# Performance work log

Measured on AMD Instinct MI355X. Metric: run time of the kernel, lower is better.

## Reference

```python
import jax, jax.numpy as jnp
import numpy as np

D = 128
H = 4
DK = D // H


def _spmm(row, col, val, x, n):
    # sparse.mm(adj, x) with adj in COO form: out[row] += val * x[col]
    return jax.ops.segment_sum(val[:, None] * x[col], row, num_segments=n)


def _arrg(h, a1_w, a1_b, a2_w, a2_b):
    return jax.nn.leaky_relu(h @ a1_w + a1_b, negative_slope=0.01) @ a2_w + a2_b


def _cross_attn(x, q_x, q_w, k_w, v_w):
    n, d = x.shape
    m = q_x.shape[0]
    q = (q_x @ q_w).reshape(m, H, DK).transpose(1, 0, 2)   # [H, Q, dk]
    k = (x @ k_w).reshape(n, H, DK).transpose(1, 0, 2)     # [H, N, dk]
    v = (q_x @ v_w).reshape(m, H, DK).transpose(1, 0, 2)   # [H, Q, dk]
    s = jnp.einsum('hnd,hqd->hnq', k, q) / jnp.sqrt(jnp.float32(DK))
    w = jax.nn.softmax(s, axis=-1)                          # softmax over queries
    out = jnp.einsum('hnq,hqd->hnd', w, v).transpose(1, 0, 2).reshape(n, d)
    return out + x


def setup_inputs() -> dict:
    key = jax.random.key(0)
    ks = iter(jax.random.split(key, 64))
    nrm = lambda shape, s=0.05: jax.random.normal(next(ks), shape, jnp.float32) * s
    inp = {}
    inp['trans_w'] = nrm((1, D)); inp['trans_b'] = nrm((D,))
    inp['g_w'] = nrm((D, D));     inp['g_b'] = nrm((D,))
    inp['qg_w'] = nrm((D, D));    inp['qg_b'] = nrm((D,))
    inp['q_w'] = nrm((D, D)); inp['k_w'] = nrm((D, D)); inp['v_w'] = nrm((D, D))
    inp['a1_w'] = nrm((D, 2 * D)); inp['a1_b'] = nrm((2 * D,))
    inp['a2_w'] = nrm((2 * D, D)); inp['a2_b'] = nrm((D,))
    inp['x0'] = jax.random.normal(next(ks), (25000,), jnp.float32)
    inp['q0'] = jax.random.normal(next(ks), (100,), jnp.float32)
    for i in (1, 2, 3):
        inp[f'xin{i}'] = jax.random.normal(next(ks), (25000,), jnp.float32)
        inp[f'qin{i}'] = jax.random.normal(next(ks), (100,), jnp.float32)
    n_sizes = {1: 50000, 2: 75000, 3: 100000}
    q_sizes = {1: 200, 2: 300, 3: 400}
    for i in (1, 2, 3):
        e = 16 * n_sizes[i]
        inp[f'aval{i}'] = jax.random.uniform(next(ks), (e,), jnp.float32)
        inp[f'arow{i}'] = jax.random.randint(next(ks), (e,), 0, n_sizes[i], jnp.int64)
        inp[f'acol{i}'] = jax.random.randint(next(ks), (e,), 0, n_sizes[i], jnp.int64)
        qe = 16 * q_sizes[i]
        inp[f'qval{i}'] = jax.random.uniform(next(ks), (qe,), jnp.float32)
        inp[f'qrow{i}'] = jax.random.randint(next(ks), (qe,), 0, q_sizes[i], jnp.int64)
        inp[f'qcol{i}'] = jax.random.randint(next(ks), (qe,), 0, q_sizes[i], jnp.int64)
    return inp


def reference(trans_w, trans_b, g_w, g_b, qg_w, qg_b, q_w, k_w, v_w,
              a1_w, a1_b, a2_w, a2_b,
              x0, q0, xin1, xin2, xin3, qin1, qin2, qin3,
              aval1, aval2, aval3, qval1, qval2, qval3,
              arow1, acol1, arow2, acol2, arow3, acol3,
              qrow1, qcol1, qrow2, qcol2, qrow3, qcol3):
    trans = lambda v: v[:, None] @ trans_w + trans_b
    x = trans(x0)
    qx = trans(q0)
    steps = [
        (xin1, qin1, arow1, acol1, aval1, qrow1, qcol1, qval1, 50000, 200),
        (xin2, qin2, arow2, acol2, aval2, qrow2, qcol2, qval2, 75000, 300),
        (xin3, qin3, arow3, acol3, aval3, qrow3, qcol3, qval3, 100000, 400),
    ]
    for xin, qin, ar, ac, av, qr, qc, qv, n, m in steps:
        x = jnp.concatenate([x, trans(xin)], axis=0)
        qx = jnp.concatenate([qx, trans(qin)], axis=0)
        x = _spmm(ar, ac, av, x @ g_w + g_b, n)
        qx = _spmm(qr, qc, qv, qx @ qg_w + qg_b, m)
        x = _arrg(x, a1_w, a1_b, a2_w, a2_b)
        qx = _arrg(qx, a1_w, a1_b, a2_w, a2_b)
        x = _cross_attn(x, qx, q_w, k_w, v_w)
    return (x, qx)
```

## Files before the change

kernel.cpp:

```cpp
#include <hip/hip_runtime.h>

typedef unsigned short u16;
typedef __attribute__((ext_vector_type(8))) short bf16x8;
typedef __attribute__((ext_vector_type(4))) float f32x4;

__device__ __forceinline__ float b2f(u16 v) {
    return __uint_as_float(((unsigned)v) << 16);
}
__device__ __forceinline__ u16 f2b(float x) {
    unsigned u = __float_as_uint(x);
    unsigned r = u + 0x7FFFu + ((u >> 16) & 1u);
    return (u16)(r >> 16);
}
__device__ __forceinline__ float4 load_bf4(const u16* p) {
    ushort4 q = *(const ushort4*)p;
    float4 f;
    f.x = b2f(q.x); f.y = b2f(q.y); f.z = b2f(q.z); f.w = b2f(q.w);
    return f;
}
__device__ __forceinline__ float4 in4(const void* p, long off, bool bf) {
    if (bf) return load_bf4((const u16*)p + off);
    return *(const float4*)((const float*)p + off);
}
__device__ __forceinline__ float in1(const void* p, long off, bool bf) {
    if (bf) return b2f(((const u16*)p)[off]);
    return ((const float*)p)[off];
}
__device__ __forceinline__ int inIdx(const void* p, long i, bool i64) {
    return ((const int*)p)[i64 ? 2 * i : i];
}

__global__ void sniff_kernel(const u16* __restrict__ x0bits, const int* __restrict__ arow,
                             int* __restrict__ flags) {
    if (threadIdx.x != 0 || blockIdx.x != 0) return;
    int plaus = 0;
    for (int i = 0; i < 256; ++i) {
        u16 v = x0bits[i];
        int e = (v >> 7) & 0xFF;
        if (v == 0 || (e >= 100 && e <= 135)) plaus++;
    }
    flags[0] = (plaus >= 200) ? 1 : 0;
    int nz = 0;
    for (int i = 1; i < 128; i += 2) nz += (arow[i] != 0);
    flags[1] = (nz == 0) ? 1 : 0;
}

__global__ void trans_kernel(const void* __restrict__ v, const void* __restrict__ tw,
                             const void* __restrict__ tb, float* __restrict__ out,
                             int rows, const int* __restrict__ flags) {
    const bool bf = flags[0] != 0;
    int t = blockIdx.x * blockDim.x + threadIdx.x;
    int c4 = (t & 31) * 4;
    int r = t >> 5;
    if (r >= rows) return;
    float vv = in1(v, r, bf);
    float4 w4 = in4(tw, c4, bf);
    float4 b4 = in4(tb, c4, bf);
    float4 o;
    o.x = vv * w4.x + b4.x; o.y = vv * w4.y + b4.y;
    o.z = vv * w4.z + b4.z; o.w = vv * w4.w + b4.w;
    *(float4*)(out + (size_t)r * 128 + c4) = o;
}

__global__ void wprep_kernel(const void* __restrict__ src, u16* __restrict__ dst,
                             int K, int N, const int* __restrict__ flags) {
    const bool bf = flags[0] != 0;
    int idx = blockIdx.x * blockDim.x + threadIdx.x;
    if (idx >= K * N) return;
    int j = idx & 7, lane = (idx >> 3) & 63, t = idx >> 9;
    int KC = K >> 5;
    int kc = t % KC, ct = t / KC;
    int k = kc * 32 + (lane >> 4) * 8 + j;
    int nn = ct * 16 + (lane & 15);
    dst[idx] = f2b(in1(src, (long)k * N + nn, bf));
}

template<int KTOT, int NOUT, bool LEAKY, typename AT, typename CT>
__launch_bounds__(256)
__global__ void gemm_mfma_kernel(const AT* __restrict__ A, const u16* __restrict__ Wf,
                                 const void* __restrict__ bias, CT* __restrict__ C,
                                 int n, const int* __restrict__ flags) {
    constexpr int KC = KTOT / 32;
    constexpr int NT = NOUT / 16;
    __shared__ u16 wlds[KTOT * NOUT];
    {
        const int4* srcw = (const int4*)Wf;
        int4* dstw = (int4*)wlds;
        constexpr int NV = KTOT * NOUT * 2 / 16;
#pragma unroll
        for (int i = 0; i < NV / 256; ++i)
            dstw[i * 256 + threadIdx.x] = srcw[i * 256 + threadIdx.x];
    }
    __syncthreads();
    const bool bf = flags[0] != 0;
    const int lane = threadIdx.x & 63;
    const int wave = threadIdx.x >> 6;
    const int quad = lane >> 4, col = lane & 15;
    const int rbase = (blockIdx.x * 4 + wave) * 16;
    if (rbase >= n) return;
    int node = rbase + col; if (node >= n) node = n - 1;
    f32x4 acc[NT];
#pragma unroll
    for (int ct = 0; ct < NT; ++ct) acc[ct] = (f32x4){0.f, 0.f, 0.f, 0.f};
#pragma unroll
    for (int kc = 0; kc < KC; ++kc) {
        bf16x8 af;
        if constexpr (sizeof(AT) == 2) {
            af = *(const bf16x8*)((const u16*)A + (size_t)node * KTOT + kc * 32 + quad * 8);
        } else {
            const float* ap = (const float*)A + (size_t)node * KTOT + kc * 32 + quad * 8;
            float4 a0 = *(const float4*)ap;
            float4 a1 = *(const float4*)(ap + 4);
            af[0] = (short)f2b(a0.x); af[1] = (short)f2b(a0.y);
            af[2] = (short)f2b(a0.z); af[3] = (short)f2b(a0.w);
            af[4] = (short)f2b(a1.x); af[5] = (short)f2b(a1.y);
            af[6] = (short)f2b(a1.z); af[7] = (short)f2b(a1.w);
        }
#pragma unroll
        for (int ct = 0; ct < NT; ++ct) {
            bf16x8 wf = *(const bf16x8*)(wlds + (((ct * KC + kc) * 64 + lane) * 8));
            acc[ct] = __builtin_amdgcn_mfma_f32_16x16x32_bf16(af, wf, acc[ct], 0, 0, 0);
        }
    }
#pragma unroll
    for (int ct = 0; ct < NT; ++ct) {
        int colg = ct * 16 + col;
        float b = bias ? in1(bias, colg, bf) : 0.f;
#pragma unroll
        for (int r = 0; r < 4; ++r) {
            int row = rbase + quad * 4 + r;
            if (row >= n) continue;
            float v = acc[ct][r] + b;
            if (LEAKY) v = v > 0.f ? v : 0.01f * v;
            if constexpr (sizeof(CT) == 2) C[(size_t)row * NOUT + colg] = (CT)f2b(v);
            else                           C[(size_t)row * NOUT + colg] = (CT)v;
        }
    }
}

#define RSH 8
#define NBC_MAX 512
#define EPB 4096

__global__ void zero_int_kernel(int* __restrict__ p, int n) {
    int i = blockIdx.x * blockDim.x + threadIdx.x;
    if (i < n) p[i] = 0;
}

__global__ void bhist_kernel(const void* __restrict__ rows, int e, int* __restrict__ bcnt,
                             int nbc, const int* __restrict__ flags) {
    __shared__ int hist[NBC_MAX];
    const bool i64 = flags[1] != 0;
    for (int i = threadIdx.x; i < nbc; i += 256) hist[i] = 0;
    __syncthreads();
    int base = blockIdx.x * 8192;
    int end = base + 8192; if (end > e) end = e;
    for (int i = base + threadIdx.x; i < end; i += 256)
        atomicAdd(&hist[inIdx(rows, i, i64) >> RSH], 1);
    __syncthreads();
    for (int i = threadIdx.x; i < nbc; i += 256) {
        int c = hist[i];
        if (c) atomicAdd(&bcnt[i], c);
    }
}

__global__ void scanA_kernel(const int* __restrict__ cnt, int n, int* __restrict__ bsum) {
    int base = blockIdx.x * 2048;
    int s = 0;
    for (int j = threadIdx.x; j < 2048; j += 256) {
        int idx = base + j;
        if (idx < n) s += cnt[idx];
    }
#pragma unroll
    for (int off = 32; off; off >>= 1) s += __shfl_down(s, off);
    __shared__ int ws[4];
    if ((threadIdx.x & 63) == 0) ws[threadIdx.x >> 6] = s;
    __syncthreads();
    if (threadIdx.x == 0) bsum[blockIdx.x] = ws[0] + ws[1] + ws[2] + ws[3];
}
__global__ void scanB_kernel(int* __restrict__ bsum, int nb) {
    if (threadIdx.x == 0) {
        int acc = 0;
        for (int i = 0; i < nb; ++i) { int v = bsum[i]; bsum[i] = acc; acc += v; }
    }
}
__global__ void scanC_kernel(const int* __restrict__ cnt, int n, const int* __restrict__ bsum,
                             int* __restrict__ optr, int* __restrict__ ocur) {
    __shared__ int tsum[256];
    int base = blockIdx.x * 2048 + threadIdx.x * 8;
    int v[8]; int s = 0;
#pragma unroll
    for (int j = 0; j < 8; ++j) {
        int idx = base + j;
        v[j] = (idx < n) ? cnt[idx] : 0;
        s += v[j];
    }
    tsum[threadIdx.x] = s;
    __syncthreads();
    for (int off = 1; off < 256; off <<= 1) {
        int t = (threadIdx.x >= off) ? tsum[threadIdx.x - off] : 0;
        __syncthreads();
        tsum[threadIdx.x] += t;
        __syncthreads();
    }
    int excl = bsum[blockIdx.x] + tsum[threadIdx.x] - s;
#pragma unroll
    for (int j = 0; j < 8; ++j) {
        int idx = base + j;
        if (idx < n) { optr[idx] = excl; ocur[idx] = excl; }
        excl += v[j];
    }
}

__launch_bounds__(256)
__global__ void psort_kernel(const void* __restrict__ rows, const void* __restrict__ colsin,
                             const void* __restrict__ valsin, int e,
                             int* __restrict__ gcur, int2* __restrict__ pack0,
                             int nbc, const int* __restrict__ flags) {
    __shared__ int hist[NBC_MAX];
    __shared__ int scan[NBC_MAX];
    __shared__ int base[NBC_MAX];
    __shared__ int cur[NBC_MAX];
    __shared__ int2 stage[EPB];
    __shared__ u16 binof[EPB];
    const bool bf = flags[0] != 0;
    const bool i64 = flags[1] != 0;
    const int tid = threadIdx.x;
    const long s0 = (long)blockIdx.x * EPB;
    int cnt_e = e - (int)s0; if (cnt_e > EPB) cnt_e = EPB;

    for (int i = tid; i < NBC_MAX; i += 256) hist[i] = 0;
    __syncthreads();
    for (int j = tid; j < cnt_e; j += 256)
        atomicAdd(&hist[inIdx(rows, s0 + j, i64) >> RSH], 1);
    __syncthreads();
    for (int i = tid; i < NBC_MAX; i += 256) scan[i] = hist[i];
    __syncthreads();
    for (int off = 1; off < NBC_MAX; off <<= 1) {
        int a = (tid >= off) ? scan[tid - off] : 0;
        int c = scan[tid + 256 - off];
        __syncthreads();
        scan[tid] += a;
        scan[tid + 256] += c;
        __syncthreads();
    }
    for (int i = tid; i < nbc; i += 256) {
        int h = hist[i];
        cur[i] = scan[i] - h;
        base[i] = h ? atomicAdd(&gcur[i], h) : 0;
    }
    __syncthreads();
    for (int j = tid; j < cnt_e; j += 256) {
        int r = inIdx(rows, s0 + j, i64);
        int bin = r >> RSH;
        int p = atomicAdd(&cur[bin], 1);
        int2 pk;
        pk.x = ((r & ((1 << RSH) - 1)) << 20) | inIdx(colsin, s0 + j, i64);
        pk.y = __float_as_int(in1(valsin, s0 + j, bf));
        stage[p] = pk;
        binof[p] = (u16)bin;
    }
    __syncthreads();
    for (int j = tid; j < cnt_e; j += 256) {
        int bin = binof[j];
        int st = scan[bin] - hist[bin];
        pack0[base[bin] + (j - st)] = stage[j];
    }
}

__launch_bounds__(256)
__global__ void breorder256_kernel(const int2* __restrict__ pack0, const int* __restrict__ bptr,
                                   const int* __restrict__ bend, int2* __restrict__ pack1,
                                   int* __restrict__ rowptr, int* __restrict__ rowend, int n) {
    __shared__ int hist[256], scan[256], cur[256];
    const int b = blockIdx.x;
    const int s = bptr[b], e = bend[b];
    const int tid = threadIdx.x;
    hist[tid] = 0;
    __syncthreads();
    for (int i = s + tid; i < e; i += 256)
        atomicAdd(&hist[(unsigned)pack0[i].x >> 20], 1);
    __syncthreads();
    scan[tid] = hist[tid];
    __syncthreads();
    for (int off = 1; off < 256; off <<= 1) {
        int a = (tid >= off) ? scan[tid - off] : 0;
        __syncthreads();
        scan[tid] += a;
        __syncthreads();
    }
    int st = s + scan[tid] - hist[tid];
    cur[tid] = st;
    int rg = (b << RSH) + tid;
    if (rg < n) { rowptr[rg] = st; rowend[rg] = st + hist[tid]; }
    __syncthreads();
    for (int i = s + tid; i < e; i += 256) {
        int2 pk = pack0[i];
        int rl = (unsigned)pk.x >> 20;
        int p = atomicAdd(&cur[rl], 1);
        pack1[p] = (int2){pk.x & 0xFFFFF, pk.y};
    }
}

__device__ __forceinline__ f32x4 bffma4(float v, uint2 h, f32x4 a) {
    a[0] += v * __uint_as_float(h.x << 16);
    a[1] += v * __uint_as_float(h.x & 0xFFFF0000u);
    a[2] += v * __uint_as_float(h.y << 16);
    a[3] += v * __uint_as_float(h.y & 0xFFFF0000u);
    return a;
}
__global__ void spmm_kernel(const u16* __restrict__ H, const int* __restrict__ rowptr,
                            const int* __restrict__ rowend, const int2* __restrict__ pack,
                            u16* __restrict__ out, int n) {
    int w = threadIdx.x >> 6;
    int lane = threadIdx.x & 63;
    int r = blockIdx.x * 4 + w;
    if (r >= n) return;
    const int half = lane >> 5;
    const int l5 = lane & 31;
    int s = rowptr[r], e = rowend[r];
    f32x4 acc = {0.f, 0.f, 0.f, 0.f};
    int i = s + half;
    for (; i + 6 < e; i += 8) {
        int2 p0 = pack[i], p1 = pack[i + 2], p2 = pack[i + 4], p3 = pack[i + 6];
        uint2 h0 = *(const uint2*)(H + (size_t)p0.x * 128 + l5 * 4);
        uint2 h1 = *(const uint2*)(H + (size_t)p1.x * 128 + l5 * 4);
        uint2 h2 = *(const uint2*)(H + (size_t)p2.x * 128 + l5 * 4);
        uint2 h3 = *(const uint2*)(H + (size_t)p3.x * 128 + l5 * 4);
        acc = bffma4(__int_as_float(p0.y), h0, acc);
        acc = bffma4(__int_as_float(p1.y), h1, acc);
        acc = bffma4(__int_as_float(p2.y), h2, acc);
        acc = bffma4(__int_as_float(p3.y), h3, acc);
    }
    for (; i < e; i += 2) {
        int2 p0 = pack[i];
        uint2 h0 = *(const uint2*)(H + (size_t)p0.x * 128 + l5 * 4);
        acc = bffma4(__int_as_float(p0.y), h0, acc);
    }
    acc[0] += __shfl_xor(acc[0], 32, 64);
    acc[1] += __shfl_xor(acc[1], 32, 64);
    acc[2] += __shfl_xor(acc[2], 32, 64);
    acc[3] += __shfl_xor(acc[3], 32, 64);
    if (half == 0) {
        ushort4 o;
        o.x = f2b(acc[0]); o.y = f2b(acc[1]); o.z = f2b(acc[2]); o.w = f2b(acc[3]);
        *(ushort4*)(out + (size_t)r * 128 + l5 * 4) = o;
    }
}

__global__ void attn_prep_kernel(const float* __restrict__ Qq, const float* __restrict__ Qv,
                                 u16* __restrict__ Qf, u16* __restrict__ Vf,
                                 int m, int mt32) {
    int idx = blockIdx.x * blockDim.x + threadIdx.x;
    int total = 4 * mt32 * 1024;
    if (idx >= total) return;
    const int mt16 = mt32 * 2;
    const float scale = 0.17677669529663687f;
    {
        int j = idx & 7, lane = (idx >> 3) & 63;
        int t = idx >> 9;
        int h = t / mt16, qt = t - h * mt16;
        int dim = ((lane >> 4) & 3) * 8 + j;
        int query = qt * 16 + (lane & 15);
        Qf[idx] = (query < m) ? f2b(Qq[(size_t)query * 128 + h * 32 + dim] * scale) : (u16)0;
    }
    {
        int j = idx & 7, lane = (idx >> 3) & 63;
        int u = idx >> 9;
        int dh = u & 1, t = u >> 1;
        int h = t / mt32, qc = t - h * mt32;
        int query = qc * 32 + ((lane >> 4) & 3) * 8 + j;
        int dim = dh * 16 + (lane & 15);
        Vf[idx] = (query < m) ? f2b(Qv[(size_t)query * 128 + h * 32 + dim]) : (u16)0;
    }
}

__launch_bounds__(256)
__global__ void attn_mfma_kernel(const u16* __restrict__ Kb, const u16* __restrict__ Qf,
                                 const u16* __restrict__ Vf, float* __restrict__ X,
                                 int n, int m, int mt32, int pad) {
    __shared__ u16 Pbuf_all[4 * 16 * 40];
    const int h = blockIdx.y;
    const int wave = threadIdx.x >> 6;
    const int lane = threadIdx.x & 63;
    u16* Pbuf = Pbuf_all + wave * 16 * 40;
    const int nb = (blockIdx.x * 4 + wave) * 16;
    if (nb >= n) return;
    const int quad = lane >> 4, col = lane & 15;
    int node = nb + col; if (node >= n) node = n - 1;
    bf16x8 kf = *(const bf16x8*)(Kb + (size_t)node * 128 + h * 32 + quad * 8);
    f32x4 O0 = {0.f, 0.f, 0.f, 0.f}, O1 = {0.f, 0.f, 0.f, 0.f};
    const f32x4 zero = {0.f, 0.f, 0.f, 0.f};
    float Lp0 = 0.f, Lp1 = 0.f, Lp2 = 0.f, Lp3 = 0.f;
    const u16* Qbase = Qf + (size_t)h * (mt32 * 2) * 512;
    const u16* Vbase = Vf + (size_t)h * mt32 * 1024;
    for (int qc = 0; qc < mt32; ++qc) {
#pragma unroll
        for (int half = 0; half < 2; ++half) {
            bf16x8 qfr = *(const bf16x8*)(Qbase + (size_t)(qc * 2 + half) * 512 + lane * 8);
            f32x4 S = __builtin_amdgcn_mfma_f32_16x16x32_bf16(kf, qfr, zero, 0, 0, 0);
            float e0 = __expf(fminf(S[0], 80.f));
            float e1 = __expf(fminf(S[1], 80.f));
            float e2 = __expf(fminf(S[2], 80.f));
            float e3 = __expf(fminf(S[3], 80.f));
            Lp0 += e0; Lp1 += e1; Lp2 += e2; Lp3 += e3;
            int qoff = half * 16 + col;
            Pbuf[(quad * 4 + 0) * 40 + qoff] = f2b(e0);
            Pbuf[(quad * 4 + 1) * 40 + qoff] = f2b(e1);
            Pbuf[(quad * 4 + 2) * 40 + qoff] = f2b(e2);
            Pbuf[(quad * 4 + 3) * 40 + qoff] = f2b(e3);
        }
        bf16x8 pf = *(const bf16x8*)(Pbuf + col * 40 + quad * 8);
        bf16x8 v0 = *(const bf16x8*)(Vbase + (size_t)(qc * 2 + 0) * 512 + lane * 8);
        bf16x8 v1 = *(const bf16x8*)(Vbase + (size_t)(qc * 2 + 1) * 512 + lane * 8);
        O0 = __builtin_amdgcn_mfma_f32_16x16x32_bf16(pf, v0, O0, 0, 0, 0);
        O1 = __builtin_amdgcn_mfma_f32_16x16x32_bf16(pf, v1, O1, 0, 0, 0);
    }
#pragma unroll
    for (int mask = 1; mask < 16; mask <<= 1) {
        Lp0 += __shfl_xor(Lp0, mask, 64);
        Lp1 += __shfl_xor(Lp1, mask, 64);
        Lp2 += __shfl_xor(Lp2, mask, 64);
        Lp3 += __shfl_xor(Lp3, mask, 64);
    }
    float inv[4];
    inv[0] = 1.f / fmaxf(Lp0 - (float)pad, 1e-35f);
    inv[1] = 1.f / fmaxf(Lp1 - (float)pad, 1e-35f);
    inv[2] = 1.f / fmaxf(Lp2 - (float)pad, 1e-35f);
    inv[3] = 1.f / fmaxf(Lp3 - (float)pad, 1e-35f);
#pragma unroll
    for (int r = 0; r < 4; ++r) {
        int nd = nb + quad * 4 + r;
        if (nd < n) {
            float* xp = X + (size_t)nd * 128 + h * 32;
            xp[col]      += O0[r] * inv[r];
            xp[16 + col] += O1[r] * inv[r];
        }
    }
}

__global__ void out_writer_kernel(const float* __restrict__ in, void* __restrict__ out,
                                  long elem_off, int n4, const int* __restrict__ flags) {
    const bool bf = flags[0] != 0;
    int i = blockIdx.x * blockDim.x + threadIdx.x;
    if (i >= n4) return;
    float4 v = ((const float4*)in)[i];
    if (bf) {
        ushort4 q; q.x = f2b(v.x); q.y = f2b(v.y); q.z = f2b(v.z); q.w = f2b(v.w);
        ((ushort4*)((u16*)out + elem_off))[i] = q;
    } else {
        ((float4*)((float*)out + elem_off))[i] = v;
    }
}

extern "C" void kernel_launch(void* const* d_in, const int* in_sizes, int n_in,
                              void* d_out, int out_size, void* d_ws, size_t ws_size,
                              hipStream_t stream) {
    (void)n_in; (void)out_size; (void)ws_size;
    const void* trans_w = d_in[0];
    const void* trans_b = d_in[1];
    const void* g_w  = d_in[2];
    const void* g_b  = d_in[3];
    const void* qg_w = d_in[4];
    const void* qg_b = d_in[5];
    const void* q_w  = d_in[6];
    const void* k_w  = d_in[7];
    const void* v_w  = d_in[8];
    const void* a1_w = d_in[9];
    const void* a1_b = d_in[10];
    const void* a2_w = d_in[11];
    const void* a2_b = d_in[12];
    const void* x0   = d_in[13];
    const void* q0   = d_in[14];

    int ixin[3], iqin[3], iaval[3], iarow[3], iacol[3], iqval[3], iqrow[3], iqcol[3];
    if (in_sizes[16] == 100) {
        for (int s = 0; s < 3; ++s) {
            ixin[s] = 15 + 2 * s; iqin[s] = 16 + 2 * s;
            int b = 21 + 6 * s;
            iaval[s] = b; iarow[s] = b + 1; iacol[s] = b + 2;
            iqval[s] = b + 3; iqrow[s] = b + 4; iqcol[s] = b + 5;
        }
    } else {
        int xs[3] = {15,16,17}, qs_[3] = {18,19,20};
        int av[3] = {21,22,23}, qv[3] = {24,25,26};
        int ar[3] = {27,29,31}, ac[3] = {28,30,32};
        int qr[3] = {33,35,37}, qc[3] = {34,36,38};
        for (int s = 0; s < 3; ++s) {
            ixin[s]=xs[s]; iqin[s]=qs_[s]; iaval[s]=av[s]; iqval[s]=qv[s];
            iarow[s]=ar[s]; iacol[s]=ac[s]; iqrow[s]=qr[s]; iqcol[s]=qc[s];
        }
    }

    char* p = (char*)d_ws;
    auto alloc = [&](size_t bytes) -> char* {
        char* r = p;
        p += (bytes + 255) & ~(size_t)255;
        return r;
    };
    int*   flags = (int*)alloc(256);
    const int NMAX = 100000;
    float* X   = (float*)alloc((size_t)NMAX * 128 * 4);
    u16*   T1b = (u16*)  alloc((size_t)NMAX * 128 * 2);
    u16*   Xs  = (u16*)  alloc((size_t)NMAX * 128 * 2);
    u16*   T2  = (u16*)  alloc((size_t)NMAX * 256 * 2);
    float* QX  = (float*)alloc((size_t)400 * 128 * 4);
    u16*   QT1b= (u16*)  alloc((size_t)400 * 128 * 2);
    u16*   QXs = (u16*)  alloc((size_t)400 * 128 * 2);
    u16*   QT2 = (u16*)  alloc((size_t)400 * 256 * 2);
    float* Qq  = (float*)alloc((size_t)400 * 128 * 4);
    float* Qv  = (float*)alloc((size_t)400 * 128 * 4);
    u16*   Qfrag = (u16*)alloc((size_t)4 * 13 * 1024 * 2);
    u16*   Vfrag = (u16*)alloc((size_t)4 * 13 * 1024 * 2);
    u16* Wg  = (u16*)alloc((size_t)128 * 128 * 2);
    u16* Wqg = (u16*)alloc((size_t)128 * 128 * 2);
    u16* Wa1 = (u16*)alloc((size_t)128 * 256 * 2);
    u16* Wa2 = (u16*)alloc((size_t)256 * 128 * 2);
    u16* Wk  = (u16*)alloc((size_t)128 * 128 * 2);
    u16* Wq  = (u16*)alloc((size_t)128 * 128 * 2);
    u16* Wv  = (u16*)alloc((size_t)128 * 128 * 2);
    int2*  csr_pack = (int2*)alloc((size_t)1600000 * 8);
    int*   bcnt   = (int*)alloc((size_t)NBC_MAX * 4);
    int*   bktptr = (int*)alloc((size_t)NBC_MAX * 4);
    int*   bktcur = (int*)alloc((size_t)NBC_MAX * 4);
    int*   rowptr = (int*)alloc((size_t)NMAX * 4);
    int*   rowend = (int*)alloc((size_t)NMAX * 4);
    int*   bsum   = (int*)alloc(256);
    int2*  pack0  = (int2*)T2;

    sniff_kernel<<<1, 64, 0, stream>>>((const u16*)x0, (const int*)d_in[iarow[0]], flags);

    auto wprep = [&](const void* src, u16* dst, int K, int N) {
        wprep_kernel<<<(K * N + 255) / 256, 256, 0, stream>>>(src, dst, K, N, flags);
    };
    wprep(g_w,  Wg,  128, 128);
    wprep(qg_w, Wqg, 128, 128);
    wprep(a1_w, Wa1, 128, 256);
    wprep(a2_w, Wa2, 256, 128);
    wprep(k_w,  Wk,  128, 128);
    wprep(q_w,  Wq,  128, 128);
    wprep(v_w,  Wv,  128, 128);

    auto launch_trans = [&](const void* v, float* out, int rows) {
        trans_kernel<<<(rows * 32 + 255) / 256, 256, 0, stream>>>(v, trans_w, trans_b, out, rows, flags);
    };
    auto build_spmm = [&](const void* rows, const void* colsidx, const void* vals, int e,
                          int nrows, const u16* H, u16* OUT) {
        int nbc = (nrows + 255) >> RSH;
        int nsb = (nbc + 2047) / 2048;
        zero_int_kernel<<<(nbc + 255) / 256, 256, 0, stream>>>(bcnt, nbc);
        bhist_kernel<<<(e + 8191) / 8192, 256, 0, stream>>>(rows, e, bcnt, nbc, flags);
        scanA_kernel<<<nsb, 256, 0, stream>>>(bcnt, nbc, bsum);
        scanB_kernel<<<1, 64, 0, stream>>>(bsum, nsb);
        scanC_kernel<<<nsb, 256, 0, stream>>>(bcnt, nbc, bsum, bktptr, bktcur);
        psort_kernel<<<(e + EPB - 1) / EPB, 256, 0, stream>>>(rows, colsidx, vals, e,
                                                              bktcur, pack0, nbc, flags);
        breorder256_kernel<<<nbc, 256, 0, stream>>>(pack0, bktptr, bktcur, csr_pack,
                                                    rowptr, rowend, nrows);
        spmm_kernel<<<(nrows + 3) / 4, 256, 0, stream>>>(H, rowptr, rowend, csr_pack,
                                                         OUT, nrows);
    };

    int nprev = in_sizes[13];
    int mprev = in_sizes[14];
    launch_trans(x0, X, nprev);
    launch_trans(q0, QX, mprev);

    const int ns[3] = {50000, 75000, 100000};
    const int ms[3] = {200, 300, 400};
    for (int s = 0; s < 3; ++s) {
        const int n = ns[s], m = ms[s];
        const int e  = in_sizes[iaval[s]];
        const int qe = in_sizes[iqval[s]];
        launch_trans(d_in[ixin[s]], X + (size_t)nprev * 128, n - nprev);
        launch_trans(d_in[iqin[s]], QX + (size_t)mprev * 128, m - mprev);
        const int gb  = (n + 63) / 64;
        const int gqb = (m + 63) / 64;
        gemm_mfma_kernel<128, 128, false, float, u16><<<gb, 256, 0, stream>>>(X, Wg, g_b, T1b, n, flags);
        build_spmm(d_in[iarow[s]], d_in[iacol[s]], d_in[iaval[s]], e, n, T1b, Xs);
        gemm_mfma_kernel<128, 128, false, float, u16><<<gqb, 256, 0, stream>>>(QX, Wqg, qg_b, QT1b, m, flags);
        build_spmm(d_in[iqrow[s]], d_in[iqcol[s]], d_in[iqval[s]], qe, m, QT1b, QXs);
        gemm_mfma_kernel<128, 256, true, u16, u16><<<gb, 256, 0, stream>>>(Xs, Wa1, a1_b, T2, n, flags);
        gemm_mfma_kernel<256, 128, false, u16, float><<<gb, 256, 0, stream>>>(T2, Wa2, a2_b, X, n, flags);
        gemm_mfma_kernel<128, 256, true, u16, u16><<<gqb, 256, 0, stream>>>(QXs, Wa1, a1_b, QT2, m, flags);
        gemm_mfma_kernel<256, 128, false, u16, float><<<gqb, 256, 0, stream>>>(QT2, Wa2, a2_b, QX, m, flags);
        gemm_mfma_kernel<128, 128, false, float, u16><<<gb, 256, 0, stream>>>(X, Wk, nullptr, T1b, n, flags);
        gemm_mfma_kernel<128, 128, false, float, float><<<gqb, 256, 0, stream>>>(QX, Wq, nullptr, Qq, m, flags);
        gemm_mfma_kernel<128, 128, false, float, float><<<gqb, 256, 0, stream>>>(QX, Wv, nullptr, Qv, m, flags);
        const int mt32 = (m + 31) / 32;
        const int pad = mt32 * 32 - m;
        const int ptot = 4 * mt32 * 1024;
        attn_prep_kernel<<<(ptot + 255) / 256, 256, 0, stream>>>(Qq, Qv, Qfrag, Vfrag, m, mt32);
        attn_mfma_kernel<<<dim3((n + 63) / 64, 4), 256, 0, stream>>>(T1b, Qfrag, Vfrag, X, n, m, mt32, pad);
        nprev = n;
        mprev = m;
    }

    const int n4x = 100000 * 128 / 4;
    const int n4q = 400 * 128 / 4;
    out_writer_kernel<<<(n4x + 255) / 256, 256, 0, stream>>>(X, d_out, 0, n4x, flags);
    out_writer_kernel<<<(n4q + 255) / 256, 256, 0, stream>>>(QX, d_out, (long)100000 * 128, n4q, flags);
}
```

Before: 1.327 ms.

## Use exp2 with folded log2e, packed bf16 stores, and transposing LDS reads in attention

Folds log2(e) into the query scale so the softmax exponent uses the native exp2 instruction instead of __expf. Replaces four scalar bf16 LDS stores per half-tile with packed v_cvt_pk_bf16_f32 conversions and one 64-bit store. The probability fragment is then read back with ds_read_b64_tr_b16 transposing loads from a new layout. This cuts ALU and LDS instruction count in the attention inner loop, at the cost of inline asm with explicit waitcnts and a sched_barrier that may hinder compiler scheduling.

Result: no change. 1.339 ms (+0.9%).

```diff
diff --git a/kernel.cpp b/kernel.cpp
--- a/kernel.cpp
+++ b/kernel.cpp
@@ -3,6 +3,7 @@
 typedef unsigned short u16;
 typedef __attribute__((ext_vector_type(8))) short bf16x8;
 typedef __attribute__((ext_vector_type(4))) float f32x4;
+typedef __attribute__((ext_vector_type(2))) unsigned u32x2;
 
 __device__ __forceinline__ float b2f(u16 v) {
     return __uint_as_float(((unsigned)v) << 16);
@@ -355,7 +356,7 @@
     int total = 4 * mt32 * 1024;
     if (idx >= total) return;
     const int mt16 = mt32 * 2;
-    const float scale = 0.17677669529663687f;
+    const float scale = 0.17677669529663687f * 1.44269504088896340736f;
     {
         int j = idx & 7, lane = (idx >> 3) & 63;
         int t = idx >> 9;
@@ -379,11 +380,10 @@
 __global__ void attn_mfma_kernel(const u16* __restrict__ Kb, const u16* __restrict__ Qf,
                                  const u16* __restrict__ Vf, float* __restrict__ X,
                                  int n, int m, int mt32, int pad) {
-    __shared__ u16 Pbuf_all[4 * 16 * 40];
+    __shared__ __align__(128) u16 Pbuf_all[4 * 512];
     const int h = blockIdx.y;
     const int wave = threadIdx.x >> 6;
     const int lane = threadIdx.x & 63;
-    u16* Pbuf = Pbuf_all + wave * 16 * 40;
     const int nb = (blockIdx.x * 4 + wave) * 16;
     if (nb >= n) return;
     const int quad = lane >> 4, col = lane & 15;
@@ -392,6 +392,11 @@
     f32x4 O0 = {0.f, 0.f, 0.f, 0.f}, O1 = {0.f, 0.f, 0.f, 0.f};
     const f32x4 zero = {0.f, 0.f, 0.f, 0.f};
     float Lp0 = 0.f, Lp1 = 0.f, Lp2 = 0.f, Lp3 = 0.f;
+    u16* Pw = Pbuf_all + wave * 512;
+    uint2* pwr[2];
+    pwr[0] = (uint2*)(Pw + col * 16 + quad * 4);
+    pwr[1] = (uint2*)(Pw + 256 + col * 16 + quad * 4);
+    const unsigned paddr = (unsigned)(uintptr_t)Pw + (unsigned)(quad * 256 + col * 8);
     const u16* Qbase = Qf + (size_t)h * (mt32 * 2) * 512;
     const u16* Vbase = Vf + (size_t)h * mt32 * 1024;
     for (int qc = 0; qc < mt32; ++qc) {
@@ -399,18 +404,26 @@
         for (int half = 0; half < 2; ++half) {
             bf16x8 qfr = *(const bf16x8*)(Qbase + (size_t)(qc * 2 + half) * 512 + lane * 8);
             f32x4 S = __builtin_amdgcn_mfma_f32_16x16x32_bf16(kf, qfr, zero, 0, 0, 0);
-            float e0 = __expf(fminf(S[0], 80.f));
-            float e1 = __expf(fminf(S[1], 80.f));
-            float e2 = __expf(fminf(S[2], 80.f));
-            float e3 = __expf(fminf(S[3], 80.f));
+            float e0 = __builtin_amdgcn_exp2f(fminf(S[0], 115.f));
+            float e1 = __builtin_amdgcn_exp2f(fminf(S[1], 115.f));
+            float e2 = __builtin_amdgcn_exp2f(fminf(S[2], 115.f));
+            float e3 = __builtin_amdgcn_exp2f(fminf(S[3], 115.f));
             Lp0 += e0; Lp1 += e1; Lp2 += e2; Lp3 += e3;
-            int qoff = half * 16 + col;
-            Pbuf[(quad * 4 + 0) * 40 + qoff] = f2b(e0);
-            Pbuf[(quad * 4 + 1) * 40 + qoff] = f2b(e1);
-            Pbuf[(quad * 4 + 2) * 40 + qoff] = f2b(e2);
-            Pbuf[(quad * 4 + 3) * 40 + qoff] = f2b(e3);
+            unsigned r01, r23;
+            asm volatile("v_cvt_pk_bf16_f32 %0, %1, %2" : "=v"(r01) : "v"(e0), "v"(e1));
+            asm volatile("v_cvt_pk_bf16_f32 %0, %1, %2" : "=v"(r23) : "v"(e2), "v"(e3));
+            uint2 pk2; pk2.x = r01; pk2.y = r23;
+            *pwr[half] = pk2;
         }
-        bf16x8 pf = *(const bf16x8*)(Pbuf + col * 40 + quad * 8);
+        asm volatile("s_waitcnt lgkmcnt(0)" ::: "memory");
+        u32x2 t0, t1;
+        asm volatile("ds_read_b64_tr_b16 %0, %1" : "=&v"(t0) : "v"(paddr) : "memory");
+        asm volatile("ds_read_b64_tr_b16 %0, %1 offset:128" : "=&v"(t1) : "v"(paddr) : "memory");
+        asm volatile("s_waitcnt lgkmcnt(0)" ::: "memory");
+        __builtin_amdgcn_sched_barrier(0);
+        bf16x8 pf;
+        ((u32x2*)&pf)[0] = t0;
+        ((u32x2*)&pf)[1] = t1;
         bf16x8 v0 = *(const bf16x8*)(Vbase + (size_t)(qc * 2 + 0) * 512 + lane * 8);
         bf16x8 v1 = *(const bf16x8*)(Vbase + (size_t)(qc * 2 + 1) * 512 + lane * 8);
         O0 = __builtin_amdgcn_mfma_f32_16x16x32_bf16(pf, v0, O0, 0, 0, 0);
```
